# Kernel tuning notes

Measured on AMD Instinct MI355X. Metric: run time of the kernel, lower is better.

The kernel has to match this reference:

```python
import jax, jax.numpy as jnp
import numpy as np

D_QUERY = 512
D_AUDIO = 512
D_OUT = 512
B, HW, S = 16, 4096, 1024


def setup_inputs() -> dict:
    key = jax.random.key(0)
    ks = jax.random.split(key, 8)
    sc_q = 1.0 / np.sqrt(D_QUERY)
    sc_a = 1.0 / np.sqrt(D_AUDIO)
    return {
        "x": jax.random.normal(ks[0], (B, HW, D_QUERY), dtype=jnp.float32),
        "audio_embed": jax.random.normal(ks[1], (B, S, D_AUDIO), dtype=jnp.float32),
        "Wq": jax.random.uniform(ks[2], (D_QUERY, D_OUT), jnp.float32, -sc_q, sc_q),
        "bq": jax.random.uniform(ks[3], (D_OUT,), jnp.float32, -sc_q, sc_q),
        "Wk": jax.random.uniform(ks[4], (D_AUDIO, D_OUT), jnp.float32, -sc_a, sc_a),
        "bk": jax.random.uniform(ks[5], (D_OUT,), jnp.float32, -sc_a, sc_a),
        "Wv": jax.random.uniform(ks[6], (D_AUDIO, D_OUT), jnp.float32, -sc_a, sc_a),
        "bv": jax.random.uniform(ks[7], (D_OUT,), jnp.float32, -sc_a, sc_a),
    }


def reference(x, audio_embed, Wq, bq, Wk, bk, Wv, bv):
    # Linear projections (nn.Linear: y = x @ W^T + b; we store W already transposed)
    Q = x @ Wq + bq                      # [B, HW, D_OUT]
    K = audio_embed @ Wk + bk            # [B, S, D_OUT]
    V = audio_embed @ Wv + bv            # [B, S, D_OUT]
    scale = 1.0 / (K.shape[-1] ** 0.5)   # divide by sqrt(d_out), per source
    scores = jnp.einsum("bnd,bsd->bns", Q, K) * scale  # [B, HW, S]
    attn = jax.nn.softmax(scores, axis=-1)
    return jnp.einsum("bns,bsd->bnd", attn, V)         # [B, HW, D_OUT]
```

## Files before the change

kernel.cpp:

```cpp
#include <hip/hip_runtime.h>
#include <hip/hip_bf16.h>

typedef __attribute__((ext_vector_type(8))) short bf16x8;
typedef __attribute__((ext_vector_type(4))) float f32x4;
typedef __attribute__((ext_vector_type(4))) unsigned short ushort4v;

#define AS1 __attribute__((address_space(1)))
#define AS3 __attribute__((address_space(3)))

__device__ __forceinline__ float bf_bits_to_f(short s) {
  unsigned int u = ((unsigned int)(unsigned short)s) << 16;
  union { unsigned int u; float f; } c; c.u = u; return c.f;
}
__device__ __forceinline__ unsigned short f_to_bf_bits(float f) {
  union { float f; unsigned int u; } c; c.f = f;
  unsigned int r = c.u + 0x7FFFu + ((c.u >> 16) & 1u);
  return (unsigned short)(r >> 16);
}

__device__ __forceinline__ int fsw(int row) { return ((row >> 1) & 3) << 4; }

__global__ __launch_bounds__(256) void cvt_bf16_kernel(const float* __restrict__ in,
                                                       unsigned short* __restrict__ out,
                                                       long n) {
  const long nchunks = n >> 2;
  const long stride = (long)gridDim.x * 256;
  for (long c = (long)blockIdx.x * 256 + threadIdx.x; c < nchunks; c += stride) {
    f32x4 v = *(const f32x4*)(in + c * 4);
    ushort4v o;
    o[0] = f_to_bf_bits(v[0]); o[1] = f_to_bf_bits(v[1]);
    o[2] = f_to_bf_bits(v[2]); o[3] = f_to_bf_bits(v[3]);
    *(ushort4v*)(out + c * 4) = o;
  }
}

__global__ __launch_bounds__(256) void transpose_w_kernel(
    const float* __restrict__ W0, const float* __restrict__ W1, const float* __restrict__ W2,
    unsigned short* __restrict__ T0, unsigned short* __restrict__ T1, unsigned short* __restrict__ T2) {
  const float* W = (blockIdx.z == 0) ? W0 : (blockIdx.z == 1) ? W1 : W2;
  unsigned short* T = (blockIdx.z == 0) ? T0 : (blockIdx.z == 1) ? T1 : T2;
  __shared__ float t[32][33];
  const int tx = threadIdx.x & 31, ty = threadIdx.x >> 5;
  const int n0 = blockIdx.x * 32, k0 = blockIdx.y * 32;
#pragma unroll
  for (int j = 0; j < 4; ++j)
    t[ty + 8 * j][tx] = W[(long)(k0 + ty + 8 * j) * 512 + n0 + tx];
  __syncthreads();
#pragma unroll
  for (int j = 0; j < 4; ++j)
    T[(long)(n0 + ty + 8 * j) * 512 + k0 + tx] = f_to_bf_bits(t[tx][ty + 8 * j]);
}

template <bool BIAS, bool TRANSOUT, bool AFP32>
__global__ __launch_bounds__(256) void gemm_kernel(
    const void* __restrict__ Aptr,
    const unsigned short* __restrict__ BT,
    const float* __restrict__ bias,
    unsigned short* __restrict__ Cout,
    const int K, const float scale,
    const long strideA, const long strideBT, const long strideC, const int ldc,
    const int nx, const int ny) {
  __shared__ unsigned short lds[8192];
  const int nwg = gridDim.x;
  const int chunk = nwg >> 3;
  const int bid = blockIdx.x;
  const int swz = (bid & 7) * chunk + (bid >> 3);
  const int bx = swz % nx;
  const int t1 = swz / nx;
  const int by = t1 % ny;
  const int bz = t1 / ny;

  const int tid = threadIdx.x;
  const int lane = tid & 63;
  const int wv = tid >> 6;
  const int wr = wv >> 1, wc = wv & 1;
  const unsigned short* Ab = (const unsigned short*)Aptr + (long)bz * strideA + (long)by * 128 * K;
  const float* Af = (const float*)Aptr + (long)bz * strideA + (long)by * 128 * K;
  const unsigned short* Bb = BT + (long)bz * strideBT + (long)bx * 128 * K;

  f32x4 acc[4][4];
#pragma unroll
  for (int m = 0; m < 4; ++m)
#pragma unroll
    for (int n = 0; n < 4; ++n) acc[m][n] = (f32x4){0.f, 0.f, 0.f, 0.f};

  const int r15 = lane & 15, g = lane >> 4;
  const int kiters = K >> 5;
  const int asw = fsw(r15);

  int arow[2], acs[2];
#pragma unroll
  for (int i = 0; i < 2; ++i) {
    const int c = i * 4 + wv;
    const int boff = c * 1024 + lane * 16;
    arow[i] = boff >> 6;
    acs[i] = (boff & 63) ^ fsw(arow[i]);
  }
  f32x4 pa[2][2];
  if (AFP32) {
#pragma unroll
    for (int i = 0; i < 2; ++i) {
      const float* s = Af + (long)arow[i] * K + (acs[i] >> 1);
      pa[i][0] = *(const f32x4*)s;
      pa[i][1] = *(const f32x4*)(s + 4);
    }
  }

  for (int kt = 0; kt < kiters; ++kt) {
#pragma unroll
    for (int i = 0; i < 2; ++i) {
      const int c = i * 4 + wv;
      const char* srcB = (const char*)Bb + (long)arow[i] * (K * 2) + kt * 64 + acs[i];
      __builtin_amdgcn_global_load_lds(
          (const AS1 void*)srcB, (AS3 void*)(lds + 4096 + c * 512), 16, 0, 0);
      if (!AFP32) {
        const char* srcA = (const char*)Ab + (long)arow[i] * (K * 2) + kt * 64 + acs[i];
        __builtin_amdgcn_global_load_lds(
            (const AS1 void*)srcA, (AS3 void*)(lds + c * 512), 16, 0, 0);
      }
    }
    if (AFP32) {
#pragma unroll
      for (int i = 0; i < 2; ++i) {
        const int c = i * 4 + wv;
        bf16x8 w;
#pragma unroll
        for (int e = 0; e < 4; ++e) {
          w[e] = (short)f_to_bf_bits(pa[i][0][e]);
          w[4 + e] = (short)f_to_bf_bits(pa[i][1][e]);
        }
        *(bf16x8*)&lds[c * 512 + lane * 8] = w;
      }
      if (kt < kiters - 1) {
#pragma unroll
        for (int i = 0; i < 2; ++i) {
          const float* s = Af + (long)arow[i] * K + (kt + 1) * 32 + (acs[i] >> 1);
          pa[i][0] = *(const f32x4*)s;
          pa[i][1] = *(const f32x4*)(s + 4);
        }
      }
    }
    __syncthreads();

    bf16x8 af[4], bf[4];
#pragma unroll
    for (int m = 0; m < 4; ++m)
      af[m] = *(const bf16x8*)((const char*)lds + (wr * 64 + m * 16 + r15) * 64 + (g * 16 ^ asw));
#pragma unroll
    for (int n = 0; n < 4; ++n)
      bf[n] = *(const bf16x8*)((const char*)lds + 8192 +
                               (wc * 64 + n * 16 + r15) * 64 + (g * 16 ^ asw));
#pragma unroll
    for (int m = 0; m < 4; ++m)
#pragma unroll
      for (int n = 0; n < 4; ++n)
        acc[m][n] = __builtin_amdgcn_mfma_f32_16x16x32_bf16(af[m], bf[n], acc[m][n], 0, 0, 0);
    __syncthreads();
  }

  const long crow0 = (long)by * 128 + wr * 64;
  const long ccol0 = (long)bx * 128 + wc * 64;
#pragma unroll
  for (int n = 0; n < 4; ++n) {
    const long col = ccol0 + n * 16 + r15;
    const float bv = BIAS ? bias[col] : 0.f;
#pragma unroll
    for (int m = 0; m < 4; ++m) {
      const f32x4 v = acc[m][n];
#pragma unroll
      for (int j = 0; j < 4; ++j) {
        const long row = crow0 + m * 16 + g * 4 + j;
        const float val = (v[j] + bv) * scale;
        const long idx = TRANSOUT ? (col * (long)ldc + row) : (row * (long)ldc + col);
        (Cout + (long)bz * strideC)[idx] = f_to_bf_bits(val);
      }
    }
  }
}

template <bool EXPSTATS, bool DIVSTATS>
__global__ __launch_bounds__(512, 2) void gemm256_kernel(
    const unsigned short* __restrict__ A,
    const unsigned short* __restrict__ BT,
    void* __restrict__ Cout,
    const int K,
    const long strideA, const long strideBT, const long strideC, const int ldc,
    const int nx, const int ny, float* __restrict__ stats) {
  __shared__ __align__(16) char halfb[4][32768];
  __shared__ float ssum[256][4];
  __shared__ float invl[256];

  const int nwg = gridDim.x;
  const int chunk = nwg >> 3;
  const int bid = blockIdx.x;
  const int swz = (bid & 7) * chunk + (bid >> 3);
  const int bx = swz % nx;
  const int t1 = swz / nx;
  const int by = t1 % ny;
  const int bz = t1 / ny;

  const int tid = threadIdx.x;
  const int lane = tid & 63;
  const int w = tid >> 6;
  const int wm = w >> 2, wn = w & 3;
  const int r15 = lane & 15, g = lane >> 4;
  const int asw = fsw(r15);

  const char* Abyt = (const char*)(A + (long)bz * strideA + (long)by * 256 * K);
  const char* Bbyt = (const char*)(BT + (long)bz * strideBT + (long)bx * 256 * K);
  const long rsb = (long)K * 2;

  if (DIVSTATS) {
    if (tid < 256) {
      const f32x4 s = *(const f32x4*)&stats[((long)bz * 4096 + (long)by * 256 + tid) * 4];
      invl[tid] = 1.f / (s[0] + s[1] + s[2] + s[3]);
    }
  }
  __builtin_amdgcn_sched_barrier(0);

  const int srow0 = tid >> 2;
  const int scol = ((tid & 3) << 4) ^ fsw(srow0);
  const long aoff0 = (long)srow0 * rsb + scol;
  const long aoff1 = (long)(srow0 + 128) * rsb + scol;
  const int dbase = tid * 16;

  auto stage = [&](int s) {
    char* h = halfb[s & 3];
    const long kb = (long)s * 64;
    __builtin_amdgcn_global_load_lds((const AS1 void*)(Abyt + aoff0 + kb),
                                     (AS3 void*)(h + dbase), 16, 0, 0);
    __builtin_amdgcn_global_load_lds((const AS1 void*)(Abyt + aoff1 + kb),
                                     (AS3 void*)(h + 8192 + dbase), 16, 0, 0);
    __builtin_amdgcn_global_load_lds((const AS1 void*)(Bbyt + aoff0 + kb),
                                     (AS3 void*)(h + 16384 + dbase), 16, 0, 0);
    __builtin_amdgcn_global_load_lds((const AS1 void*)(Bbyt + aoff1 + kb),
                                     (AS3 void*)(h + 24576 + dbase), 16, 0, 0);
  };

  f32x4 acc[8][4];
#pragma unroll
  for (int m = 0; m < 8; ++m)
#pragma unroll
    for (int n = 0; n < 4; ++n) acc[m][n] = (f32x4){0.f, 0.f, 0.f, 0.f};

  const int kslices = K >> 5;

  stage(0);
  stage(1);
  stage(2);
  asm volatile("s_waitcnt vmcnt(8)" ::: "memory");
  __builtin_amdgcn_s_barrier();
  __builtin_amdgcn_sched_barrier(0);

  for (int s = 0; s < kslices; ++s) {
    const char* hA = halfb[s & 3];
    const char* hB = halfb[s & 3] + 16384;
    bf16x8 fa[8], fb[4];
#pragma unroll
    for (int m = 0; m < 8; ++m)
      fa[m] = *(const bf16x8*)(hA + (wm * 128 + m * 16 + r15) * 64 + ((g * 16) ^ asw));
#pragma unroll
    for (int n = 0; n < 4; ++n)
      fb[n] = *(const bf16x8*)(hB + (wn * 64 + n * 16 + r15) * 64 + ((g * 16) ^ asw));
    __builtin_amdgcn_sched_barrier(0);
    if (s < kslices - 2) asm volatile("s_waitcnt vmcnt(4)" ::: "memory");
    else                 asm volatile("s_waitcnt vmcnt(0)" ::: "memory");
    __builtin_amdgcn_s_barrier();
    asm volatile("s_waitcnt lgkmcnt(0)" ::: "memory");
    __builtin_amdgcn_sched_barrier(0);
    if (s + 3 < kslices) stage(s + 3);
    __builtin_amdgcn_s_setprio(1);
#pragma unroll
    for (int m = 0; m < 8; ++m)
#pragma unroll
      for (int n = 0; n < 4; ++n)
        acc[m][n] = __builtin_amdgcn_mfma_f32_16x16x32_bf16(fa[m], fb[n], acc[m][n], 0, 0, 0);
    __builtin_amdgcn_s_setprio(0);
    __builtin_amdgcn_sched_barrier(0);
  }

  if (EXPSTATS) {
#pragma unroll
    for (int m = 0; m < 8; ++m)
#pragma unroll
      for (int n = 0; n < 4; ++n)
#pragma unroll
        for (int j = 0; j < 4; ++j) acc[m][n][j] = __expf(acc[m][n][j]);
#pragma unroll
    for (int m = 0; m < 8; ++m)
#pragma unroll
      for (int j = 0; j < 4; ++j) {
        float s = acc[m][0][j] + acc[m][1][j] + acc[m][2][j] + acc[m][3][j];
        s += __shfl_xor(s, 1);
        s += __shfl_xor(s, 2);
        s += __shfl_xor(s, 4);
        s += __shfl_xor(s, 8);
        if (r15 == 0) ssum[wm * 128 + m * 16 + g * 4 + j][wn] = s;
      }
    __syncthreads();
    if (tid < 256) {
      const float t = ssum[tid][0] + ssum[tid][1] + ssum[tid][2] + ssum[tid][3];
      stats[((long)bz * 4096 + (long)by * 256 + tid) * 4 + bx] = t;
    }
  }

  const long crow0 = (long)by * 256 + wm * 128;
  const long ccol0 = (long)bx * 256 + wn * 64;
#pragma unroll
  for (int m = 0; m < 8; ++m)
#pragma unroll
    for (int j = 0; j < 4; ++j) {
      const int rl = wm * 128 + m * 16 + g * 4 + j;
      const long row = crow0 + m * 16 + g * 4 + j;
#pragma unroll
      for (int n = 0; n < 4; ++n) {
        const long col = ccol0 + n * 16 + r15;
        if (EXPSTATS) {
          ((unsigned short*)Cout + (long)bz * strideC)[row * (long)ldc + col] =
              f_to_bf_bits(acc[m][n][j]);
        } else {
          const float sc = DIVSTATS ? invl[rl] : 1.f;
          ((float*)Cout + (long)bz * strideC)[row * (long)ldc + col] = acc[m][n][j] * sc;
        }
      }
    }
}

extern "C" void kernel_launch(void* const* d_in, const int* in_sizes, int n_in,
                              void* d_out, int out_size, void* d_ws, size_t ws_size,
                              hipStream_t stream) {
  (void)in_sizes; (void)n_in; (void)out_size; (void)ws_size;
  const float* x     = (const float*)d_in[0];
  const float* audio = (const float*)d_in[1];
  const float* Wq    = (const float*)d_in[2];
  const float* bq    = (const float*)d_in[3];
  const float* Wk    = (const float*)d_in[4];
  const float* bk    = (const float*)d_in[5];
  const float* Wv    = (const float*)d_in[6];
  const float* bv    = (const float*)d_in[7];
  float* out = (float*)d_out;

  char* ws = (char*)d_ws;
  size_t off = 0;
  auto carve = [&](size_t bytes) { char* p = ws + off; off += (bytes + 255) & ~(size_t)255; return p; };
  unsigned short* ab  = (unsigned short*)carve((size_t)16384 * 512 * 2);
  unsigned short* wqt = (unsigned short*)carve((size_t)512 * 512 * 2);
  unsigned short* wkt = (unsigned short*)carve((size_t)512 * 512 * 2);
  unsigned short* wvt = (unsigned short*)carve((size_t)512 * 512 * 2);
  unsigned short* Qb  = (unsigned short*)carve((size_t)65536 * 512 * 2);
  unsigned short* Kb  = (unsigned short*)carve((size_t)16384 * 512 * 2);
  unsigned short* Vt  = (unsigned short*)carve((size_t)16384 * 512 * 2);
  unsigned short* Pb  = (unsigned short*)carve((size_t)65536 * 1024 * 2);
  float*          ls  = (float*)carve((size_t)65536 * 4 * 4);

  cvt_bf16_kernel<<<1024, 256, 0, stream>>>(audio, ab, (long)16384 * 512);
  transpose_w_kernel<<<dim3(16, 16, 3), 256, 0, stream>>>(Wq, Wk, Wv, wqt, wkt, wvt);
  gemm_kernel<true, false, true><<<4 * 512, 256, 0, stream>>>(
      x, wqt, bq, Qb, 512, 0.044194173824159216f, 0, 0, 0, 512, 4, 512);
  gemm_kernel<true, false, false><<<4 * 128, 256, 0, stream>>>(
      ab, wkt, bk, Kb, 512, 1.f, 0, 0, 0, 512, 4, 128);
  gemm_kernel<true, true, false><<<4 * 8 * 16, 256, 0, stream>>>(
      ab, wvt, bv, Vt, 512, 1.f, (long)1024 * 512, 0, (long)512 * 1024, 1024, 4, 8);
  gemm256_kernel<true, false><<<4 * 16 * 16, 512, 0, stream>>>(
      Qb, Kb, Pb, 512,
      (long)4096 * 512, (long)1024 * 512, (long)4096 * 1024, 1024, 4, 16, ls);
  gemm256_kernel<false, true><<<2 * 16 * 16, 512, 0, stream>>>(
      Pb, Vt, out, 1024,
      (long)4096 * 1024, (long)512 * 1024, (long)4096 * 512, 512, 2, 16, ls);
}
```

Before: 337.3 us.

## Fold Q projection into K via Wq·Wk^T, dropping the large Q GEMM

Scores are rewritten algebraically as x·(Wq·Wkᵀ)·audioᵀ plus a per-key bias from bq·Wkᵀ·audio. Terms constant along the softmax row (those involving bk) are dropped because softmax ignores them. This removes the 65536x512x512 Q projection GEMM and replaces it with a bf16 conversion of x, a small 512x512 weight product, and a projection of the smaller audio tensor. The tradeoff is more bf16 rounding through the fused G matrix, a few extra small kernel launches, and a full-size bf16 copy of x.

```diff
diff --git a/kernel.cpp b/kernel.cpp
--- a/kernel.cpp
+++ b/kernel.cpp
@@ -34,11 +34,8 @@
   }
 }
 
-__global__ __launch_bounds__(256) void transpose_w_kernel(
-    const float* __restrict__ W0, const float* __restrict__ W1, const float* __restrict__ W2,
-    unsigned short* __restrict__ T0, unsigned short* __restrict__ T1, unsigned short* __restrict__ T2) {
-  const float* W = (blockIdx.z == 0) ? W0 : (blockIdx.z == 1) ? W1 : W2;
-  unsigned short* T = (blockIdx.z == 0) ? T0 : (blockIdx.z == 1) ? T1 : T2;
+__global__ __launch_bounds__(256) void transpose1_kernel(
+    const float* __restrict__ W, unsigned short* __restrict__ T) {
   __shared__ float t[32][33];
   const int tx = threadIdx.x & 31, ty = threadIdx.x >> 5;
   const int n0 = blockIdx.x * 32, k0 = blockIdx.y * 32;
@@ -49,6 +46,39 @@
 #pragma unroll
   for (int j = 0; j < 4; ++j)
     T[(long)(n0 + ty + 8 * j) * 512 + k0 + tx] = f_to_bf_bits(t[tx][ty + 8 * j]);
+}
+
+__global__ __launch_bounds__(256) void wvec_kernel(const float* __restrict__ Wk,
+                                                   const float* __restrict__ bq,
+                                                   float* __restrict__ w, const float s) {
+  const int q = blockIdx.x * 4 + (threadIdx.x >> 6);
+  const int lane = threadIdx.x & 63;
+  const float* row = Wk + (long)q * 512 + lane * 8;
+  const f32x4 a0 = *(const f32x4*)row;
+  const f32x4 a1 = *(const f32x4*)(row + 4);
+  const f32x4 b0 = *(const f32x4*)(bq + lane * 8);
+  const f32x4 b1 = *(const f32x4*)(bq + lane * 8 + 4);
+  float d = a0[0]*b0[0] + a0[1]*b0[1] + a0[2]*b0[2] + a0[3]*b0[3]
+          + a1[0]*b1[0] + a1[1]*b1[1] + a1[2]*b1[2] + a1[3]*b1[3];
+  for (int off = 1; off < 64; off <<= 1) d += __shfl_xor(d, off);
+  if (lane == 0) w[q] = d * s;
+}
+
+__global__ __launch_bounds__(256) void cvec_kernel(const unsigned short* __restrict__ ab,
+                                                   const float* __restrict__ w,
+                                                   float* __restrict__ cv) {
+  const long row = (long)blockIdx.x * 4 + (threadIdx.x >> 6);
+  const int lane = threadIdx.x & 63;
+  const bf16x8 a = *(const bf16x8*)(ab + row * 512 + lane * 8);
+  const f32x4 w0 = *(const f32x4*)(w + lane * 8);
+  const f32x4 w1 = *(const f32x4*)(w + lane * 8 + 4);
+  float d = 0.f;
+#pragma unroll
+  for (int e = 0; e < 4; ++e) d += bf_bits_to_f(a[e]) * w0[e];
+#pragma unroll
+  for (int e = 0; e < 4; ++e) d += bf_bits_to_f(a[4 + e]) * w1[e];
+  for (int off = 1; off < 64; off <<= 1) d += __shfl_xor(d, off);
+  if (lane == 0) cv[row] = d;
 }
 
 template <bool BIAS, bool TRANSOUT, bool AFP32>
@@ -185,7 +215,8 @@
     void* __restrict__ Cout,
     const int K,
     const long strideA, const long strideBT, const long strideC, const int ldc,
-    const int nx, const int ny, float* __restrict__ stats) {
+    const int nx, const int ny, float* __restrict__ stats,
+    const float* __restrict__ cbias) {
   __shared__ __align__(16) char halfb[4][32768];
   __shared__ float ssum[256][4];
   __shared__ float invl[256];
@@ -280,12 +311,16 @@
   }
 
   if (EXPSTATS) {
+    float cb[4];
+#pragma unroll
+    for (int n = 0; n < 4; ++n)
+      cb[n] = cbias[(long)bz * 1024 + (long)bx * 256 + wn * 64 + n * 16 + r15];
 #pragma unroll
     for (int m = 0; m < 8; ++m)
 #pragma unroll
       for (int n = 0; n < 4; ++n)
 #pragma unroll
-        for (int j = 0; j < 4; ++j) acc[m][n][j] = __expf(acc[m][n][j]);
+        for (int j = 0; j < 4; ++j) acc[m][n][j] = __expf(acc[m][n][j] + cb[n]);
 #pragma unroll
     for (int m = 0; m < 8; ++m)
 #pragma unroll
@@ -335,36 +370,44 @@
   const float* Wq    = (const float*)d_in[2];
   const float* bq    = (const float*)d_in[3];
   const float* Wk    = (const float*)d_in[4];
-  const float* bk    = (const float*)d_in[5];
+  const float* bk    = (const float*)d_in[5];  (void)bk;
   const float* Wv    = (const float*)d_in[6];
   const float* bv    = (const float*)d_in[7];
   float* out = (float*)d_out;
 
+  const float s = 0.044194173824159216f;
+
   char* ws = (char*)d_ws;
   size_t off = 0;
   auto carve = [&](size_t bytes) { char* p = ws + off; off += (bytes + 255) & ~(size_t)255; return p; };
+  unsigned short* xb  = (unsigned short*)carve((size_t)65536 * 512 * 2);
   unsigned short* ab  = (unsigned short*)carve((size_t)16384 * 512 * 2);
-  unsigned short* wqt = (unsigned short*)carve((size_t)512 * 512 * 2);
-  unsigned short* wkt = (unsigned short*)carve((size_t)512 * 512 * 2);
+  unsigned short* wkb = (unsigned short*)carve((size_t)512 * 512 * 2);
   unsigned short* wvt = (unsigned short*)carve((size_t)512 * 512 * 2);
-  unsigned short* Qb  = (unsigned short*)carve((size_t)65536 * 512 * 2);
-  unsigned short* Kb  = (unsigned short*)carve((size_t)16384 * 512 * 2);
+  unsigned short* G   = (unsigned short*)carve((size_t)512 * 512 * 2);
+  unsigned short* KMb = (unsigned short*)carve((size_t)16384 * 512 * 2);
   unsigned short* Vt  = (unsigned short*)carve((size_t)16384 * 512 * 2);
   unsigned short* Pb  = (unsigned short*)carve((size_t)65536 * 1024 * 2);
   float*          ls  = (float*)carve((size_t)65536 * 4 * 4);
-
+  float*          wv_ = (float*)carve((size_t)512 * 4);
+  float*          cv  = (float*)carve((size_t)16384 * 4);
+
+  cvt_bf16_kernel<<<2048, 256, 0, stream>>>(x, xb, (long)65536 * 512);
   cvt_bf16_kernel<<<1024, 256, 0, stream>>>(audio, ab, (long)16384 * 512);
-  transpose_w_kernel<<<dim3(16, 16, 3), 256, 0, stream>>>(Wq, Wk, Wv, wqt, wkt, wvt);
-  gemm_kernel<true, false, true><<<4 * 512, 256, 0, stream>>>(
-      x, wqt, bq, Qb, 512, 0.044194173824159216f, 0, 0, 0, 512, 4, 512);
-  gemm_kernel<true, false, false><<<4 * 128, 256, 0, stream>>>(
-      ab, wkt, bk, Kb, 512, 1.f, 0, 0, 0, 512, 4, 128);
+  cvt_bf16_kernel<<<256, 256, 0, stream>>>(Wk, wkb, (long)512 * 512);
+  transpose1_kernel<<<dim3(16, 16), 256, 0, stream>>>(Wv, wvt);
+  gemm_kernel<false, false, true><<<16, 256, 0, stream>>>(
+      Wq, wkb, nullptr, G, 512, s, 0, 0, 0, 512, 4, 4);
+  wvec_kernel<<<128, 256, 0, stream>>>(Wk, bq, wv_, s);
+  cvec_kernel<<<4096, 256, 0, stream>>>(ab, wv_, cv);
   gemm_kernel<true, true, false><<<4 * 8 * 16, 256, 0, stream>>>(
       ab, wvt, bv, Vt, 512, 1.f, (long)1024 * 512, 0, (long)512 * 1024, 1024, 4, 8);
+  gemm_kernel<false, false, false><<<4 * 8 * 16, 256, 0, stream>>>(
+      ab, G, nullptr, KMb, 512, 1.f, (long)1024 * 512, 0, (long)1024 * 512, 512, 4, 8);
   gemm256_kernel<true, false><<<4 * 16 * 16, 512, 0, stream>>>(
-      Qb, Kb, Pb, 512,
-      (long)4096 * 512, (long)1024 * 512, (long)4096 * 1024, 1024, 4, 16, ls);
+      xb, KMb, Pb, 512,
+      (long)4096 * 512, (long)1024 * 512, (long)4096 * 1024, 1024, 4, 16, ls, cv);
   gemm256_kernel<false, true><<<2 * 16 * 16, 512, 0, stream>>>(
       Pb, Vt, out, 1024,
-      (long)4096 * 1024, (long)512 * 1024, (long)4096 * 512, 512, 2, 16, ls);
-}
+      (long)4096 * 1024, (long)512 * 1024, (long)4096 * 512, 512, 2, 16, ls, nullptr);
+}
```

Measured after the change: 328.5 us. 2.6% less time.
